# Kernel optimization log

Hardware: AMD Instinct MI355X
Metric: run time of the kernel (lower is better)

Reference implementation:

```python
import jax, jax.numpy as jnp
import numpy as np
import math

NUM_HEADS = 8
RES_K = 9  # res_kernel_size


def setup_inputs() -> dict:
    key = jax.random.key(0)
    ks = jax.random.split(key, 6)
    N, C, h, w = 8, 256, 64, 64
    x = jax.random.normal(ks[0], (N, C, h, w), dtype=jnp.float32)
    w_qkv = jax.random.normal(ks[1], (3 * C, C), dtype=jnp.float32) * 0.02
    b_qkv = jax.random.normal(ks[2], (3 * C,), dtype=jnp.float32) * 0.02
    w_proj = jax.random.normal(ks[3], (C, C), dtype=jnp.float32) * 0.02
    b_proj = jax.random.normal(ks[4], (C,), dtype=jnp.float32) * 0.02
    w_dconv = jax.random.normal(ks[5], (NUM_HEADS, 1, RES_K, 1), dtype=jnp.float32) * 0.1
    return {"x": x, "w_qkv": w_qkv, "b_qkv": b_qkv,
            "w_proj": w_proj, "b_proj": b_proj, "w_dconv": w_dconv}


def _l2norm(t):
    # torch x / x.norm(dim=-1, keepdim=True): plain L2 norm, no eps
    return t / jnp.linalg.norm(t, axis=-1, keepdims=True)


def reference(x, w_qkv, b_qkv, w_proj, b_proj, w_dconv):
    N, C, h, w = x.shape
    H = NUM_HEADS
    D = C // H
    L = h * w
    xt = x.reshape(N, C, L).transpose(0, 2, 1)  # [N, L, C]
    qkv = xt @ w_qkv.T + b_qkv                   # [N, L, 3C]
    qkv = qkv.reshape(N, L, 3, H, D).transpose(2, 0, 3, 1, 4)  # [3, N, H, L, D]
    q, k, v = qkv[0], qkv[1], qkv[2]
    q = _l2norm(q)
    k = _l2norm(k)
    # depthwise conv over token dim: v as NCHW with C=H, H=L, W=D
    pad = RES_K // 2
    dconv_v = jax.lax.conv_general_dilated(
        v, w_dconv, window_strides=(1, 1), padding=[(pad, pad), (0, 0)],
        dimension_numbers=("NCHW", "OIHW", "NCHW"), feature_group_count=H)
    attn = jnp.einsum("nhld,nhle->nhde", k, v)   # [N, H, D, D]
    out = 0.5 * v + (1.0 / math.pi) * jnp.einsum("nhld,nhde->nhle", q, attn)
    out = _l2norm(out)
    out = out + dconv_v
    out = out.transpose(0, 2, 1, 3).reshape(N, L, C)  # [N, L, C]
    out = out @ w_proj.T + b_proj
    return out.transpose(0, 2, 1).reshape(N, C, h, w)
```

## Files before the change

### kernel.cpp

```cpp
#include <hip/hip_runtime.h>

#define NB 8
#define CC 256
#define HH 8
#define DD 32
#define LL 4096

typedef short v8s __attribute__((ext_vector_type(8)));
typedef float v4f __attribute__((ext_vector_type(4)));
typedef unsigned short v8u __attribute__((ext_vector_type(8)));
typedef unsigned short v4us __attribute__((ext_vector_type(4)));

__device__ __forceinline__ float4 ld4(const float* p) { return *(const float4*)p; }

__device__ __forceinline__ unsigned short f2bf(float f) {
    union { float f; unsigned int u; } v; v.f = f;
    unsigned int r = (v.u + 0x7FFFu + ((v.u >> 16) & 1u)) >> 16;
    return (unsigned short)r;
}
__device__ __forceinline__ float bf2f(unsigned short u) {
    union { unsigned int u; float f; } v; v.u = ((unsigned int)u) << 16;
    return v.f;
}

__device__ __forceinline__ void gl_lds16(const unsigned short* g, unsigned short* l) {
    __builtin_amdgcn_global_load_lds(
        (const __attribute__((address_space(1))) void*)g,
        (__attribute__((address_space(3))) void*)l, 16, 0, 0);
}

__global__ __launch_bounds__(256) void prep_w(
    const float* __restrict__ wq, const float* __restrict__ wp,
    unsigned short* __restrict__ dwq, unsigned short* __restrict__ dwp)
{
    int ti = blockIdx.x * 256 + threadIdx.x;
    if (ti < 24576) {
        int i = ti * 8;
        float4 f0 = ld4(wq + i), f1 = ld4(wq + i + 4);
        v8u o;
        o[0] = f2bf(f0.x); o[1] = f2bf(f0.y); o[2] = f2bf(f0.z); o[3] = f2bf(f0.w);
        o[4] = f2bf(f1.x); o[5] = f2bf(f1.y); o[6] = f2bf(f1.z); o[7] = f2bf(f1.w);
        *(v8u*)(dwq + i) = o;
    } else {
        int i = (ti - 24576) * 8;
        float4 f0 = ld4(wp + i), f1 = ld4(wp + i + 4);
        v8u o;
        o[0] = f2bf(f0.x); o[1] = f2bf(f0.y); o[2] = f2bf(f0.z); o[3] = f2bf(f0.w);
        o[4] = f2bf(f1.x); o[5] = f2bf(f1.y); o[6] = f2bf(f1.z); o[7] = f2bf(f1.w);
        *(v8u*)(dwp + i) = o;
    }
}

__global__ __launch_bounds__(256, 2) void gemm_qkv_mfma(
    const float* __restrict__ x, const unsigned short* __restrict__ wqb,
    const float* __restrict__ bqkv,
    unsigned short* __restrict__ q, unsigned short* __restrict__ k,
    unsigned short* __restrict__ v, float* __restrict__ attn)
{
    __shared__ __align__(16) unsigned short xs[8192];
    __shared__ __align__(16) unsigned short wsb[16384];

    const int bid  = blockIdx.x;
    const int xcd  = bid & 7;
    const int slot = bid >> 3;
    const int jt   = slot % 3;
    const int p    = slot / 3;
    const int gp   = xcd * 32 + p;
    const int l0   = (gp & 31) * 128;
    const int n    = gp >> 5;
    const int j0   = jt * 256;

    const int tid = threadIdx.x;
    const int lane = tid & 63, wave = tid >> 6;
    const int wr = wave >> 1, wc = wave & 1;
    const int r = lane & 15, quad = lane >> 4;

    if (jt == 2) attn[gp * 256 + tid] = 0.f;

    const int srow = wave * 8 + (lane >> 3);
    const int dchunk = (lane & 7) ^ (lane >> 3);
    const unsigned short* wg = wqb + (size_t)(j0 + srow) * CC + dchunk * 8;
    unsigned short* wls = wsb + wave * 512 + lane * 8;

    const int lw = tid & 127;
    const int half = tid >> 7;
    const float* xrow = x + (size_t)n * CC * LL + l0 + lw;

    v4f acc[8][4];
#pragma unroll
    for (int mi = 0; mi < 8; ++mi)
#pragma unroll
        for (int nj = 0; nj < 4; ++nj) acc[mi][nj] = (v4f)(0.f);

    const int jbase = wr * 128;
    const int lbase = wc * 64;

    for (int kt = 0; kt < 4; ++kt) {
        if (kt) __syncthreads();
        const int c0 = kt * 64;
#pragma unroll
        for (int i = 0; i < 8; ++i)
            gl_lds16(wg + (size_t)i * 32 * CC + c0, wls + i * 2048);
#pragma unroll
        for (int chi = 0; chi < 4; ++chi) {
            int ch = half * 4 + chi;
            const float* src = xrow + (size_t)(c0 + ch * 8) * LL;
            float f[8];
#pragma unroll
            for (int j = 0; j < 8; ++j) f[j] = src[(size_t)j * LL];
            v8u o;
#pragma unroll
            for (int j = 0; j < 8; ++j) o[j] = f2bf(f[j]);
            *(v8u*)(xs + lw * 64 + ((ch ^ (lw & 7)) * 8)) = o;
        }
        __syncthreads();

#pragma unroll
        for (int kk = 0; kk < 2; ++kk) {
            const int cfrag = kk * 4 + quad;
            const int s = cfrag ^ (r & 7);
            v8s b[4];
#pragma unroll
            for (int nj = 0; nj < 4; ++nj) {
                int lloc = lbase + nj * 16 + r;
                b[nj] = *(const v8s*)(xs + lloc * 64 + s * 8);
            }
            v8s a[8];
#pragma unroll
            for (int mi = 0; mi < 8; ++mi) {
                int jloc = jbase + mi * 16 + r;
                a[mi] = *(const v8s*)(wsb + jloc * 64 + s * 8);
            }
#pragma unroll
            for (int mi = 0; mi < 8; ++mi)
#pragma unroll
                for (int nj = 0; nj < 4; ++nj)
                    acc[mi][nj] = __builtin_amdgcn_mfma_f32_16x16x32_bf16(
                        a[mi], b[nj], acc[mi][nj], 0, 0, 0);
        }
    }

    unsigned short* base = (jt == 0 ? q : (jt == 1 ? k : v));

    float bias[8][4];
#pragma unroll
    for (int mi = 0; mi < 8; ++mi)
        *(float4*)bias[mi] = *(const float4*)(bqkv + j0 + jbase + mi * 16 + quad * 4);

    unsigned short* dstp[8];
#pragma unroll
    for (int mi = 0; mi < 8; ++mi) {
        int hh = wr * 4 + (mi >> 1);
        int d0 = (mi & 1) * 16 + quad * 4;
        dstp[mi] = base + (size_t)(n * HH + hh) * LL * DD + d0;
    }

    if (jt < 2) {
#pragma unroll
        for (int nj = 0; nj < 4; ++nj) {
            float t[8][4];
            float ss[4] = {0.f, 0.f, 0.f, 0.f};
#pragma unroll
            for (int mi = 0; mi < 8; ++mi)
#pragma unroll
                for (int reg = 0; reg < 4; ++reg) {
                    float val = acc[mi][nj][reg] + bias[mi][reg];
                    t[mi][reg] = val;
                    ss[mi >> 1] += val * val;
                }
#pragma unroll
            for (int h4 = 0; h4 < 4; ++h4) {
                ss[h4] += __shfl_xor(ss[h4], 16);
                ss[h4] += __shfl_xor(ss[h4], 32);
                ss[h4] = rsqrtf(ss[h4]);
            }
            size_t l = (size_t)(l0 + lbase + nj * 16 + r);
#pragma unroll
            for (int mi = 0; mi < 8; ++mi) {
                float rn = ss[mi >> 1];
                v4us pk;
#pragma unroll
                for (int reg = 0; reg < 4; ++reg) pk[reg] = f2bf(t[mi][reg] * rn);
                *(v4us*)(dstp[mi] + l * DD) = pk;
            }
        }
    } else {
#pragma unroll
        for (int nj = 0; nj < 4; ++nj) {
            size_t l = (size_t)(l0 + lbase + nj * 16 + r);
#pragma unroll
            for (int mi = 0; mi < 8; ++mi) {
                v4us pk;
#pragma unroll
                for (int reg = 0; reg < 4; ++reg)
                    pk[reg] = f2bf(acc[mi][nj][reg] + bias[mi][reg]);
                *(v4us*)(dstp[mi] + l * DD) = pk;
            }
        }
    }
}

__global__ __launch_bounds__(256) void attn_k(
    const unsigned short* __restrict__ k, const unsigned short* __restrict__ v,
    float* __restrict__ attn)
{
    __shared__ float red[4][1024];
    const int nh = blockIdx.y;
    const int wv = threadIdx.x >> 6;
    const int lane = threadIdx.x & 63;
    const int eg = lane & 7;
    const int dg = lane >> 3;
    const int l0 = blockIdx.x * 512 + wv * 128;
    const unsigned short* kb = k + (size_t)nh * LL * DD;
    const unsigned short* vb = v + (size_t)nh * LL * DD;
    float acc[4][4] = {};
#pragma unroll 4
    for (int l = l0; l < l0 + 128; ++l) {
        v4us k4 = *(const v4us*)(kb + (size_t)l * DD + dg * 4);
        v4us v4 = *(const v4us*)(vb + (size_t)l * DD + eg * 4);
        float ka[4] = {bf2f(k4[0]), bf2f(k4[1]), bf2f(k4[2]), bf2f(k4[3])};
        float va[4] = {bf2f(v4[0]), bf2f(v4[1]), bf2f(v4[2]), bf2f(v4[3])};
#pragma unroll
        for (int dp = 0; dp < 4; ++dp)
#pragma unroll
            for (int ep = 0; ep < 4; ++ep)
                acc[dp][ep] += ka[dp] * va[ep];
    }
#pragma unroll
    for (int dp = 0; dp < 4; ++dp)
#pragma unroll
        for (int ep = 0; ep < 4; ++ep)
            red[wv][(dg * 4 + dp) * 32 + eg * 4 + ep] = acc[dp][ep];
    __syncthreads();
    float* ap = attn + (size_t)nh * 1024;
    for (int i = threadIdx.x; i < 1024; i += 256)
        atomicAdd(&ap[i], red[0][i] + red[1][i] + red[2][i] + red[3][i]);
}

#define PTOK 64
#define VTP 40
__global__ __launch_bounds__(256, 2) void midproj_k(
    const unsigned short* __restrict__ q, const unsigned short* __restrict__ v,
    const float* __restrict__ attn, const float* __restrict__ wd,
    const unsigned short* __restrict__ wpb, const float* __restrict__ bp,
    float* __restrict__ out)
{
    __shared__ __align__(16) unsigned short vt[8 * 72 * VTP];
    __shared__ __align__(16) unsigned short smid[4 * 64 * 64];

    const int n  = blockIdx.y;
    const int l0 = blockIdx.x * PTOK;
    const int tid = threadIdx.x;
    const int lane = tid & 63, wave = tid >> 6;
    const int r = lane & 15, quad = lane >> 4;

    const unsigned short* vbase = v + (size_t)(n * HH) * LL * DD;
#pragma unroll
    for (int it = 0; it < 9; ++it) {
        int task = it * 256 + tid;
        int seg = task & 3;
        int hr = task >> 2;
        int row = hr % 72;
        int h = hr / 72;
        int l = l0 - 4 + row;
        v8u val;
        if (l >= 0 && l < LL)
            val = *(const v8u*)(vbase + ((size_t)h * LL + l) * DD + seg * 8);
        else
            val = (v8u)(unsigned short)0;
        *(v8u*)(&vt[hr * VTP + seg * 8]) = val;
    }
    __syncthreads();

    const float inv_pi = 0.31830988618379067f;
#pragma unroll
    for (int hi = 0; hi < 2; ++hi) {
        const int h = wave * 2 + hi;
        const int nh = n * HH + h;
        const unsigned short* qb = q + (size_t)nh * LL * DD;
        const unsigned short* vth = vt + h * 72 * VTP;

        v8s bfrag[2];
#pragma unroll
        for (int et = 0; et < 2; ++et) {
            int e = et * 16 + r;
#pragma unroll
            for (int j = 0; j < 8; ++j)
                ((unsigned short*)&bfrag[et])[j] =
                    f2bf(attn[(size_t)nh * 1024 + (quad * 8 + j) * 32 + e]);
        }
        float wc[9];
#pragma unroll
        for (int r9 = 0; r9 < 9; ++r9) wc[r9] = wd[h * 9 + r9];

#pragma unroll
        for (int lt = 0; lt < 4; ++lt) {
            const int tb = lt * 16;
            v8s afrag = *(const v8s*)(qb + (size_t)(l0 + tb + r) * DD + quad * 8);
            v4f acc[2] = {(v4f)(0.f), (v4f)(0.f)};
#pragma unroll
            for (int et = 0; et < 2; ++et)
                acc[et] = __builtin_amdgcn_mfma_f32_16x16x32_bf16(
                    afrag, bfrag[et], acc[et], 0, 0, 0);

            float vcol[2][12];
#pragma unroll
            for (int et = 0; et < 2; ++et) {
                int e = et * 16 + r;
#pragma unroll
                for (int o = 0; o < 12; ++o)
                    vcol[et][o] = bf2f(vth[(tb + quad * 4 + o) * VTP + e]);
            }

            float t[2][4], ss[4];
#pragma unroll
            for (int reg = 0; reg < 4; ++reg) {
                t[0][reg] = 0.5f * vcol[0][4 + reg] + inv_pi * acc[0][reg];
                t[1][reg] = 0.5f * vcol[1][4 + reg] + inv_pi * acc[1][reg];
                ss[reg] = t[0][reg] * t[0][reg] + t[1][reg] * t[1][reg];
            }
#pragma unroll
            for (int m = 1; m < 16; m <<= 1)
#pragma unroll
                for (int reg = 0; reg < 4; ++reg)
                    ss[reg] += __shfl_xor(ss[reg], m);
#pragma unroll
            for (int reg = 0; reg < 4; ++reg) ss[reg] = rsqrtf(ss[reg]);

#pragma unroll
            for (int et = 0; et < 2; ++et) {
                int c = h * 32 + et * 16 + r;
                int chunk = c >> 6, c6 = c & 63;
                int goff = c6 & 7;
#pragma unroll
                for (int reg = 0; reg < 4; ++reg) {
                    float dv = 0.f;
#pragma unroll
                    for (int r9 = 0; r9 < 9; ++r9) dv += wc[r9] * vcol[et][reg + r9];
                    int l = tb + quad * 4 + reg;
                    int g = (c6 >> 3) ^ (l & 7);
                    smid[chunk * 4096 + l * 64 + g * 8 + goff] =
                        f2bf(t[et][reg] * ss[reg] + dv);
                }
            }
        }
    }
    __syncthreads();

    const int jbase = wave * 64;
    v4f acc[4][4];
#pragma unroll
    for (int mi = 0; mi < 4; ++mi)
#pragma unroll
        for (int nj = 0; nj < 4; ++nj) acc[mi][nj] = (v4f)(0.f);

#pragma unroll
    for (int kt = 0; kt < 4; ++kt) {
        v8s a[4][2], b[4][2];
#pragma unroll
        for (int kk = 0; kk < 2; ++kk) {
            const int cfrag = kk * 4 + quad;
#pragma unroll
            for (int mi = 0; mi < 4; ++mi) {
                int j = jbase + mi * 16 + r;
                a[mi][kk] = *(const v8s*)(wpb + (size_t)j * CC + kt * 64 + cfrag * 8);
            }
            const int s = cfrag ^ (r & 7);
#pragma unroll
            for (int nj = 0; nj < 4; ++nj) {
                int lloc = nj * 16 + r;
                b[nj][kk] = *(const v8s*)(smid + kt * 4096 + lloc * 64 + s * 8);
            }
        }
#pragma unroll
        for (int kk = 0; kk < 2; ++kk)
#pragma unroll
            for (int mi = 0; mi < 4; ++mi)
#pragma unroll
                for (int nj = 0; nj < 4; ++nj)
                    acc[mi][nj] = __builtin_amdgcn_mfma_f32_16x16x32_bf16(
                        a[mi][kk], b[nj][kk], acc[mi][nj], 0, 0, 0);
    }

#pragma unroll
    for (int mi = 0; mi < 4; ++mi)
#pragma unroll
        for (int reg = 0; reg < 4; ++reg) {
            int j = jbase + mi * 16 + quad * 4 + reg;
            float bias = bp[j];
#pragma unroll
            for (int nj = 0; nj < 4; ++nj) {
                int l = l0 + nj * 16 + r;
                out[((size_t)n * CC + j) * LL + l] = acc[mi][nj][reg] + bias;
            }
        }
}

extern "C" void kernel_launch(void* const* d_in, const int* in_sizes, int n_in,
                              void* d_out, int out_size, void* d_ws, size_t ws_size,
                              hipStream_t stream)
{
    const float* x     = (const float*)d_in[0];
    const float* wqkv  = (const float*)d_in[1];
    const float* bqkv  = (const float*)d_in[2];
    const float* wproj = (const float*)d_in[3];
    const float* bproj = (const float*)d_in[4];
    const float* wd    = (const float*)d_in[5];
    float* out = (float*)d_out;

    const size_t QKV = (size_t)NB * HH * LL * DD;
    unsigned short* q = (unsigned short*)d_ws;
    unsigned short* k = q + QKV;
    unsigned short* v = k + QKV;
    float* attn = (float*)(v + QKV);
    unsigned short* wqb = (unsigned short*)(attn + (size_t)NB * HH * DD * DD);
    unsigned short* wpb = wqb + 3 * CC * CC;

    prep_w<<<128, 256, 0, stream>>>(wqkv, wproj, wqb, wpb);
    gemm_qkv_mfma<<<768, 256, 0, stream>>>(x, wqb, bqkv, q, k, v, attn);
    attn_k<<<dim3(8, 64), 256, 0, stream>>>(k, v, attn);
    midproj_k<<<dim3(LL / PTOK, NB), 256, 0, stream>>>(q, v, attn, wd, wpb, bproj, out);
}
```

Measured before the change: 158.9 us.

## Load x tile once per block and loop over q/k/v output slices

The QKV GEMM now gives each block a 64-token tile with the full 256-channel x slice staged in LDS as bf16. The block loops over the three 256-column weight slices (q, k, v), so x is read from global memory and converted only once instead of three times across blocks. In exchange, LDS use grows, the grid shrinks from 768 to 512 blocks, each wave's tile is smaller (4x4 MFMA tiles), and the XCD-aware block mapping is removed. Weight tiles are still loaded per k-step, with an extra barrier.

```diff
diff --git a/kernel.cpp b/kernel.cpp
--- a/kernel.cpp
+++ b/kernel.cpp
@@ -57,144 +57,133 @@
     unsigned short* __restrict__ q, unsigned short* __restrict__ k,
     unsigned short* __restrict__ v, float* __restrict__ attn)
 {
-    __shared__ __align__(16) unsigned short xs[8192];
+    __shared__ __align__(16) unsigned short xsf[16384];
     __shared__ __align__(16) unsigned short wsb[16384];
 
-    const int bid  = blockIdx.x;
-    const int xcd  = bid & 7;
-    const int slot = bid >> 3;
-    const int jt   = slot % 3;
-    const int p    = slot / 3;
-    const int gp   = xcd * 32 + p;
-    const int l0   = (gp & 31) * 128;
-    const int n    = gp >> 5;
-    const int j0   = jt * 256;
-
+    const int bid = blockIdx.x;
+    const int l0 = (bid & 63) * 64;
+    const int n  = bid >> 6;
     const int tid = threadIdx.x;
     const int lane = tid & 63, wave = tid >> 6;
-    const int wr = wave >> 1, wc = wave & 1;
     const int r = lane & 15, quad = lane >> 4;
 
-    if (jt == 2) attn[gp * 256 + tid] = 0.f;
+    if (bid < 256) attn[bid * 256 + tid] = 0.f;
+
+    {
+        const int lx = tid & 63, cq = tid >> 6;
+        const float* xcol = x + (size_t)n * CC * LL + l0 + lx;
+        unsigned short* xrow = xsf + lx * 256;
+#pragma unroll
+        for (int i = 0; i < 8; ++i) {
+            const float* src = xcol + (size_t)(cq * 8 + i) * 8 * LL;
+            float f[8];
+#pragma unroll
+            for (int j = 0; j < 8; ++j) f[j] = src[(size_t)j * LL];
+            v8u o;
+#pragma unroll
+            for (int j = 0; j < 8; ++j) o[j] = f2bf(f[j]);
+            *(v8u*)(xrow + (cq * 8 + (i ^ (lx & 7))) * 8) = o;
+        }
+    }
 
     const int srow = wave * 8 + (lane >> 3);
     const int dchunk = (lane & 7) ^ (lane >> 3);
-    const unsigned short* wg = wqb + (size_t)(j0 + srow) * CC + dchunk * 8;
     unsigned short* wls = wsb + wave * 512 + lane * 8;
-
-    const int lw = tid & 127;
-    const int half = tid >> 7;
-    const float* xrow = x + (size_t)n * CC * LL + l0 + lw;
-
-    v4f acc[8][4];
-#pragma unroll
-    for (int mi = 0; mi < 8; ++mi)
-#pragma unroll
-        for (int nj = 0; nj < 4; ++nj) acc[mi][nj] = (v4f)(0.f);
-
-    const int jbase = wr * 128;
-    const int lbase = wc * 64;
-
-    for (int kt = 0; kt < 4; ++kt) {
-        if (kt) __syncthreads();
-        const int c0 = kt * 64;
-#pragma unroll
-        for (int i = 0; i < 8; ++i)
-            gl_lds16(wg + (size_t)i * 32 * CC + c0, wls + i * 2048);
-#pragma unroll
-        for (int chi = 0; chi < 4; ++chi) {
-            int ch = half * 4 + chi;
-            const float* src = xrow + (size_t)(c0 + ch * 8) * LL;
-            float f[8];
-#pragma unroll
-            for (int j = 0; j < 8; ++j) f[j] = src[(size_t)j * LL];
-            v8u o;
-#pragma unroll
-            for (int j = 0; j < 8; ++j) o[j] = f2bf(f[j]);
-            *(v8u*)(xs + lw * 64 + ((ch ^ (lw & 7)) * 8)) = o;
-        }
-        __syncthreads();
-
-#pragma unroll
-        for (int kk = 0; kk < 2; ++kk) {
-            const int cfrag = kk * 4 + quad;
-            const int s = cfrag ^ (r & 7);
-            v8s b[4];
+    const int jbase = wave * 64;
+
+    for (int jt = 0; jt < 3; ++jt) {
+        const int j0 = jt * 256;
+        const unsigned short* wg = wqb + (size_t)(j0 + srow) * CC + dchunk * 8;
+
+        v4f acc[4][4];
+#pragma unroll
+        for (int mi = 0; mi < 4; ++mi)
+#pragma unroll
+            for (int nj = 0; nj < 4; ++nj) acc[mi][nj] = (v4f)(0.f);
+
+        for (int kt = 0; kt < 4; ++kt) {
+            __syncthreads();
+#pragma unroll
+            for (int i = 0; i < 8; ++i)
+                gl_lds16(wg + (size_t)i * 32 * CC + kt * 64, wls + i * 2048);
+            __syncthreads();
+
+#pragma unroll
+            for (int kk = 0; kk < 2; ++kk) {
+                const int cfrag = kk * 4 + quad;
+                const int s = cfrag ^ (r & 7);
+                v8s b[4];
+#pragma unroll
+                for (int nj = 0; nj < 4; ++nj)
+                    b[nj] = *(const v8s*)(xsf + (nj * 16 + r) * 256 + kt * 64 + s * 8);
+                v8s a[4];
+#pragma unroll
+                for (int mi = 0; mi < 4; ++mi)
+                    a[mi] = *(const v8s*)(wsb + (jbase + mi * 16 + r) * 64 + s * 8);
+#pragma unroll
+                for (int mi = 0; mi < 4; ++mi)
+#pragma unroll
+                    for (int nj = 0; nj < 4; ++nj)
+                        acc[mi][nj] = __builtin_amdgcn_mfma_f32_16x16x32_bf16(
+                            a[mi], b[nj], acc[mi][nj], 0, 0, 0);
+            }
+        }
+
+        unsigned short* basep = (jt == 0 ? q : (jt == 1 ? k : v));
+        float bias[4][4];
+#pragma unroll
+        for (int mi = 0; mi < 4; ++mi)
+            *(float4*)bias[mi] = *(const float4*)(bqkv + j0 + jbase + mi * 16 + quad * 4);
+
+        unsigned short* dstp[4];
+#pragma unroll
+        for (int mi = 0; mi < 4; ++mi) {
+            int hh = wave * 2 + (mi >> 1);
+            int d0 = (mi & 1) * 16 + quad * 4;
+            dstp[mi] = basep + (size_t)(n * HH + hh) * LL * DD + d0;
+        }
+
+        if (jt < 2) {
 #pragma unroll
             for (int nj = 0; nj < 4; ++nj) {
-                int lloc = lbase + nj * 16 + r;
-                b[nj] = *(const v8s*)(xs + lloc * 64 + s * 8);
-            }
-            v8s a[8];
-#pragma unroll
-            for (int mi = 0; mi < 8; ++mi) {
-                int jloc = jbase + mi * 16 + r;
-                a[mi] = *(const v8s*)(wsb + jloc * 64 + s * 8);
-            }
-#pragma unroll
-            for (int mi = 0; mi < 8; ++mi)
-#pragma unroll
-                for (int nj = 0; nj < 4; ++nj)
-                    acc[mi][nj] = __builtin_amdgcn_mfma_f32_16x16x32_bf16(
-                        a[mi], b[nj], acc[mi][nj], 0, 0, 0);
-        }
-    }
-
-    unsigned short* base = (jt == 0 ? q : (jt == 1 ? k : v));
-
-    float bias[8][4];
-#pragma unroll
-    for (int mi = 0; mi < 8; ++mi)
-        *(float4*)bias[mi] = *(const float4*)(bqkv + j0 + jbase + mi * 16 + quad * 4);
-
-    unsigned short* dstp[8];
-#pragma unroll
-    for (int mi = 0; mi < 8; ++mi) {
-        int hh = wr * 4 + (mi >> 1);
-        int d0 = (mi & 1) * 16 + quad * 4;
-        dstp[mi] = base + (size_t)(n * HH + hh) * LL * DD + d0;
-    }
-
-    if (jt < 2) {
-#pragma unroll
-        for (int nj = 0; nj < 4; ++nj) {
-            float t[8][4];
-            float ss[4] = {0.f, 0.f, 0.f, 0.f};
-#pragma unroll
-            for (int mi = 0; mi < 8; ++mi)
-#pragma unroll
-                for (int reg = 0; reg < 4; ++reg) {
-                    float val = acc[mi][nj][reg] + bias[mi][reg];
-                    t[mi][reg] = val;
-                    ss[mi >> 1] += val * val;
+                float t[4][4];
+                float ss[2] = {0.f, 0.f};
+#pragma unroll
+                for (int mi = 0; mi < 4; ++mi)
+#pragma unroll
+                    for (int reg = 0; reg < 4; ++reg) {
+                        float val = acc[mi][nj][reg] + bias[mi][reg];
+                        t[mi][reg] = val;
+                        ss[mi >> 1] += val * val;
+                    }
+#pragma unroll
+                for (int g2 = 0; g2 < 2; ++g2) {
+                    ss[g2] += __shfl_xor(ss[g2], 16);
+                    ss[g2] += __shfl_xor(ss[g2], 32);
+                    ss[g2] = rsqrtf(ss[g2]);
                 }
-#pragma unroll
-            for (int h4 = 0; h4 < 4; ++h4) {
-                ss[h4] += __shfl_xor(ss[h4], 16);
-                ss[h4] += __shfl_xor(ss[h4], 32);
-                ss[h4] = rsqrtf(ss[h4]);
-            }
-            size_t l = (size_t)(l0 + lbase + nj * 16 + r);
-#pragma unroll
-            for (int mi = 0; mi < 8; ++mi) {
-                float rn = ss[mi >> 1];
-                v4us pk;
-#pragma unroll
-                for (int reg = 0; reg < 4; ++reg) pk[reg] = f2bf(t[mi][reg] * rn);
-                *(v4us*)(dstp[mi] + l * DD) = pk;
-            }
-        }
-    } else {
-#pragma unroll
-        for (int nj = 0; nj < 4; ++nj) {
-            size_t l = (size_t)(l0 + lbase + nj * 16 + r);
-#pragma unroll
-            for (int mi = 0; mi < 8; ++mi) {
-                v4us pk;
-#pragma unroll
-                for (int reg = 0; reg < 4; ++reg)
-                    pk[reg] = f2bf(acc[mi][nj][reg] + bias[mi][reg]);
-                *(v4us*)(dstp[mi] + l * DD) = pk;
+                size_t l = (size_t)(l0 + nj * 16 + r);
+#pragma unroll
+                for (int mi = 0; mi < 4; ++mi) {
+                    float rn = ss[mi >> 1];
+                    v4us pk;
+#pragma unroll
+                    for (int reg = 0; reg < 4; ++reg) pk[reg] = f2bf(t[mi][reg] * rn);
+                    *(v4us*)(dstp[mi] + l * DD) = pk;
+                }
+            }
+        } else {
+#pragma unroll
+            for (int nj = 0; nj < 4; ++nj) {
+                size_t l = (size_t)(l0 + nj * 16 + r);
+#pragma unroll
+                for (int mi = 0; mi < 4; ++mi) {
+                    v4us pk;
+#pragma unroll
+                    for (int reg = 0; reg < 4; ++reg)
+                        pk[reg] = f2bf(acc[mi][nj][reg] + bias[mi][reg]);
+                    *(v4us*)(dstp[mi] + l * DD) = pk;
+                }
             }
         }
     }
@@ -417,7 +406,7 @@
     unsigned short* wpb = wqb + 3 * CC * CC;
 
     prep_w<<<128, 256, 0, stream>>>(wqkv, wproj, wqb, wpb);
-    gemm_qkv_mfma<<<768, 256, 0, stream>>>(x, wqb, bqkv, q, k, v, attn);
+    gemm_qkv_mfma<<<512, 256, 0, stream>>>(x, wqb, bqkv, q, k, v, attn);
     attn_k<<<dim3(8, 64), 256, 0, stream>>>(k, v, attn);
     midproj_k<<<dim3(LL / PTOK, NB), 256, 0, stream>>>(q, v, attn, wd, wpb, bproj, out);
 }
```

Result: faster. 150.3 us (-5.4%).
